# Performance work log

Hardware: AMD Instinct MI355X
Metric: run time of the kernel (lower is better)

## Reference

```python
import jax, jax.numpy as jnp
import numpy as np

B, S, D, H, F = 2, 2048, 1024, 16, 4096
DK = D // H
EPS = 1e-6


def _ln(x, g, b):
    mu = jnp.mean(x, axis=-1, keepdims=True)
    var = jnp.mean(jnp.square(x - mu), axis=-1, keepdims=True)
    return (x - mu) * jax.lax.rsqrt(var + EPS) * g + b


def setup_inputs() -> dict:
    key = jax.random.key(0)
    ks = jax.random.split(key, 8)
    sc = 0.02
    return {
        "x": jax.random.normal(ks[0], (B, S, D), jnp.float32),
        "wq": jax.random.normal(ks[1], (D, D), jnp.float32) * sc,
        "bq": jnp.zeros((D,), jnp.float32),
        "wk": jax.random.normal(ks[2], (D, D), jnp.float32) * sc,
        "bk": jnp.zeros((D,), jnp.float32),
        "wv": jax.random.normal(ks[3], (D, D), jnp.float32) * sc,
        "bv": jnp.zeros((D,), jnp.float32),
        "wo": jax.random.normal(ks[4], (D, D), jnp.float32) * sc,
        "bo": jnp.zeros((D,), jnp.float32),
        "w1": jax.random.normal(ks[5], (D, F), jnp.float32) * sc,
        "b1": jnp.zeros((F,), jnp.float32),
        "w2": jax.random.normal(ks[6], (F, D), jnp.float32) * sc,
        "b2": jnp.zeros((D,), jnp.float32),
        "g1": jnp.ones((D,), jnp.float32),
        "be1": jnp.zeros((D,), jnp.float32),
        "g2": jnp.ones((D,), jnp.float32),
        "be2": jnp.zeros((D,), jnp.float32),
    }


def reference(x, wq, bq, wk, bk, wv, bv, wo, bo, w1, b1, w2, b2, g1, be1, g2, be2):
    # Multi-head self-attention (no masks, eval-mode dropout = identity)
    q = (x @ wq + bq).reshape(B, S, H, DK)
    k = (x @ wk + bk).reshape(B, S, H, DK)
    v = (x @ wv + bv).reshape(B, S, H, DK)
    scale = 1.0 / (DK ** 0.5)
    score = jnp.einsum('bihd,bjhd->bhij', q, k) * scale  # [B,H,S,S]
    p = jax.nn.softmax(score, axis=-1)
    attn = jnp.einsum('bhij,bjhd->bihd', p, v).reshape(B, S, D)
    attn = attn @ wo + bo
    # residual + LayerNorm 1
    h = _ln(x + attn, g1, be1)
    # FFN (relu) + residual + LayerNorm 2
    ff = jax.nn.relu(h @ w1 + b1) @ w2 + b2
    return _ln(h + ff, g2, be2)
```

## Files before the change

### kernel.cpp

```cpp
#include <hip/hip_runtime.h>
#include <hip/hip_bf16.h>
#include <cmath>

typedef __bf16 bf16_t;
typedef __bf16 bf16x4 __attribute__((ext_vector_type(4)));
typedef __bf16 bf16x8 __attribute__((ext_vector_type(8)));
typedef float  f32x4  __attribute__((ext_vector_type(4)));

__device__ __forceinline__ void gld_lds16(const bf16_t* g, bf16_t* l) {
    __builtin_amdgcn_global_load_lds(
        (const __attribute__((address_space(1))) void*)g,
        (__attribute__((address_space(3))) void*)l,
        16, 0, 0);
}

struct PrepArgs {
    const float* w[6]; bf16_t* wt[6];
    int K[6], N[6], start[6];
    const float* x; bf16_t* xb; int castStart;
    const float* bq; const float* bk; float* bqkv; int biasStart;
};

__global__ __launch_bounds__(256) void prep(PrepArgs pa) {
    __shared__ float tile[32][33];
    const int bid = blockIdx.x, t = threadIdx.x;
    if (bid < pa.castStart) {
        int mi = 0;
#pragma unroll
        for (int i = 1; i < 6; i++) if (bid >= pa.start[i]) mi = i;
        const int tt  = bid - pa.start[mi];
        const int nbx = pa.N[mi] >> 5;
        const int n0 = (tt % nbx) * 32, k0 = (tt / nbx) * 32;
        const float* in = pa.w[mi];
        bf16_t* out = pa.wt[mi];
        const int K = pa.K[mi], N = pa.N[mi];
        const int tx = t & 31, ty = t >> 5;
#pragma unroll
        for (int i = 0; i < 4; i++) {
            int kk = ty + i * 8;
            tile[kk][tx] = in[(size_t)(k0 + kk) * N + n0 + tx];
        }
        __syncthreads();
#pragma unroll
        for (int i = 0; i < 4; i++) {
            int nn = ty + i * 8;
            out[(size_t)(n0 + nn) * K + k0 + tx] = (bf16_t)tile[tx][nn];
        }
    } else if (bid < pa.biasStart) {
        int i = (bid - pa.castStart) * 256 + t;
        f32x4 v = ((const f32x4*)pa.x)[i];
        bf16x4 o;
        o[0] = (bf16_t)v[0]; o[1] = (bf16_t)v[1]; o[2] = (bf16_t)v[2]; o[3] = (bf16_t)v[3];
        ((bf16x4*)pa.xb)[i] = o;
    } else {
#pragma unroll
        for (int j = 0; j < 8; j++) {
            int idx = t * 8 + j;
            pa.bqkv[idx] = idx < 1024 ? pa.bq[idx] : pa.bk[idx - 1024];
        }
    }
}

template<int MT>
__global__ __launch_bounds__(256) void gemm_bt(
    const bf16_t* __restrict__ A, const bf16_t* __restrict__ Bt,
    const float* __restrict__ bias,
    float* __restrict__ Cf, bf16_t* __restrict__ Cb,
    int M, int N, int lda, int Kloc, int relu, int nbn, int bias_row,
    long bt_bstride, long c_bstride) {
    constexpr int TM = MT * 32;
    __shared__ __attribute__((aligned(16))) bf16_t As[2][TM * 32];
    __shared__ __attribute__((aligned(16))) bf16_t Bs[2][128 * 32];
    const int tid  = threadIdx.x;
    const int lane = tid & 63;
    const int wave = tid >> 6;
    const int wm = wave & 1, wn = wave >> 1;
    const int kh = blockIdx.z;

    const int span  = 8 * nbn;
    const int group = blockIdx.x / span;
    const int rem   = blockIdx.x % span;
    const int bm    = group * 8 + (rem & 7);
    const int bn    = rem >> 3;

    const bf16_t* Bt_b = Bt + (size_t)blockIdx.y * bt_bstride;
    float*  Cf_b = Cf ? Cf + (size_t)blockIdx.y * c_bstride + (size_t)kh * M * N : nullptr;
    bf16_t* Cb_b = Cb ? Cb + (size_t)blockIdx.y * c_bstride : nullptr;
    const int koff = kh * Kloc;

    const int r4 = tid >> 2;
    const int kc = (tid & 3) * 8;
    const bf16_t* Ag = A    + (size_t)(bm * TM  + r4) * lda + koff + kc;
    const bf16_t* Bg = Bt_b + (size_t)(bn * 128 + r4) * lda + koff + kc;

    f32x4 acc[MT][4] = {};
    const int mrow = lane & 15;
    const int q8   = (lane >> 4) * 8;

    for (int k0 = 0; k0 < Kloc; k0 += 64) {
        __syncthreads();
#pragma unroll
        for (int hh = 0; hh < 2; hh++) {
#pragma unroll
            for (int i = 0; i < MT / 2; i++)
                gld_lds16(Ag + (size_t)(i * 64) * lda + k0 + hh * 32,
                          &As[hh][i * 64 * 32] + tid * 8);
            gld_lds16(Bg + k0 + hh * 32,                  &Bs[hh][0] + tid * 8);
            gld_lds16(Bg + (size_t)64 * lda + k0 + hh * 32, &Bs[hh][64 * 32] + tid * 8);
        }
        __syncthreads();

#pragma unroll
        for (int hh = 0; hh < 2; hh++) {
            bf16x8 af[MT], bfr[4];
#pragma unroll
            for (int mt = 0; mt < MT; mt++)
                af[mt] = *(const bf16x8*)(&As[hh][(wm * (MT * 16) + mt * 16 + mrow) * 32 + q8]);
#pragma unroll
            for (int nt = 0; nt < 4; nt++)
                bfr[nt] = *(const bf16x8*)(&Bs[hh][(wn * 64 + nt * 16 + mrow) * 32 + q8]);
#pragma unroll
            for (int mt = 0; mt < MT; mt++)
#pragma unroll
                for (int nt = 0; nt < 4; nt++)
                    acc[mt][nt] = __builtin_amdgcn_mfma_f32_16x16x32_bf16(
                        af[mt], bfr[nt], acc[mt][nt], 0, 0, 0);
        }
    }

    const int rq = (lane >> 4) * 4;
#pragma unroll
    for (int mt = 0; mt < MT; mt++) {
        int row0 = bm * TM + wm * (MT * 16) + mt * 16 + rq;
#pragma unroll
        for (int nt = 0; nt < 4; nt++) {
            int col = bn * 128 + wn * 64 + nt * 16 + mrow;
            float bvc = (bias && kh == 0 && !bias_row) ? bias[col] : 0.f;
#pragma unroll
            for (int r = 0; r < 4; r++) {
                float bb = (bias && kh == 0 && bias_row) ? bias[row0 + r] : bvc;
                float v = acc[mt][nt][r] + bb;
                if (relu) v = fmaxf(v, 0.f);
                size_t idx = (size_t)(row0 + r) * N + col;
                if (Cf_b) Cf_b[idx] = v;
                if (Cb_b) Cb_b[idx] = (bf16_t)v;
            }
        }
    }
}

__global__ __launch_bounds__(256) void flash_attn_mfma(
    const bf16_t* __restrict__ QKb,
    const bf16_t* __restrict__ Vtg,
    bf16_t* __restrict__ Outb) {
    __shared__ __attribute__((aligned(16))) bf16_t Ks[2][4096];
    __shared__ __attribute__((aligned(16))) bf16_t Vs[2][4096];
    __shared__ __attribute__((aligned(16))) bf16_t Ps[4096];
    const int t = threadIdx.x;
    const int lane = t & 63, wave = t >> 6;
    const int g = lane >> 4, cl = lane & 15;
    const int b = blockIdx.z, h = blockIdx.y, q0 = blockIdx.x * 64;
    const int RS = 2048;
    const bf16_t* Qg = QKb + (size_t)(b * 2048 + q0) * RS + h * 64;
    const bf16_t* Kg = QKb + (size_t)(b * 2048) * RS + 1024 + h * 64;
    const bf16_t* Vg = Vtg + ((size_t)b * 1024 + h * 64) * 2048;

    const int sr = t >> 2;
    const int sc = (t & 3) * 8;

    const bf16_t* Qrow = Qg + (size_t)(wave * 16 + cl) * RS;
    bf16x8 qr0 = *(const bf16x8*)(Qrow + g * 8);
    bf16x8 qr1 = *(const bf16x8*)(Qrow + 32 + g * 8);

    gld_lds16(Kg + (size_t)sr * RS + sc,        &Ks[0][0]    + t * 8);
    gld_lds16(Kg + (size_t)sr * RS + 32 + sc,   &Ks[0][2048] + t * 8);
    gld_lds16(Vg + (size_t)sr * 2048 + sc,      &Vs[0][0]    + t * 8);
    gld_lds16(Vg + (size_t)sr * 2048 + 32 + sc, &Vs[0][2048] + t * 8);
    __syncthreads();

    f32x4 Oacc[4] = {};
    f32x4 Lacc = {};
    bf16x8 ones;
#pragma unroll
    for (int j = 0; j < 8; j++) ones[j] = (bf16_t)1.0f;

    const int rowb = wave * 16 + cl;
    const int psw  = (cl & 7) << 4;
    char* PsB = (char*)Ps;
    const float C = 0.125f * 1.4426950408889634f;

    for (int kt_i = 0; kt_i < 32; ++kt_i) {
        const int cur = kt_i & 1;
        if (kt_i + 1 < 32) {
            const int nb  = cur ^ 1;
            const int ktn = (kt_i + 1) * 64;
            gld_lds16(Kg + (size_t)(ktn + sr) * RS + sc,        &Ks[nb][0]    + t * 8);
            gld_lds16(Kg + (size_t)(ktn + sr) * RS + 32 + sc,   &Ks[nb][2048] + t * 8);
            gld_lds16(Vg + (size_t)sr * 2048 + ktn + sc,        &Vs[nb][0]    + t * 8);
            gld_lds16(Vg + (size_t)sr * 2048 + ktn + 32 + sc,   &Vs[nb][2048] + t * 8);
        }

        f32x4 Sacc[4] = {};
#pragma unroll
        for (int ks = 0; ks < 2; ++ks) {
            bf16x8 bq = ks ? qr1 : qr0;
#pragma unroll
            for (int mt = 0; mt < 4; ++mt) {
                bf16x8 ak = *(const bf16x8*)(&Ks[cur][ks * 2048 + (mt * 16 + cl) * 32 + g * 8]);
                Sacc[mt] = __builtin_amdgcn_mfma_f32_16x16x32_bf16(ak, bq, Sacc[mt], 0, 0, 0);
            }
        }

#pragma unroll
        for (int mt = 0; mt < 4; ++mt) {
            bf16x4 p4;
#pragma unroll
            for (int r = 0; r < 4; r++)
                p4[r] = (bf16_t)__builtin_amdgcn_exp2f(Sacc[mt][r] * C);
            *(bf16x4*)(PsB + ((rowb * 128 + mt * 32 + g * 8) ^ psw)) = p4;
        }

#pragma unroll
        for (int ks = 0; ks < 2; ++ks) {
            bf16x8 ap = *(const bf16x8*)(PsB + ((rowb * 128 + ks * 64 + g * 16) ^ psw));
            Lacc = __builtin_amdgcn_mfma_f32_16x16x32_bf16(ap, ones, Lacc, 0, 0, 0);
#pragma unroll
            for (int nt = 0; nt < 4; ++nt) {
                bf16x8 bv = *(const bf16x8*)(&Vs[cur][ks * 2048 + (nt * 16 + cl) * 32 + g * 8]);
                Oacc[nt] = __builtin_amdgcn_mfma_f32_16x16x32_bf16(ap, bv, Oacc[nt], 0, 0, 0);
            }
        }

        __syncthreads();
    }

#pragma unroll
    for (int r = 0; r < 4; r++) {
        float inv = 1.f / Lacc[r];
        int qrow = q0 + wave * 16 + g * 4 + r;
        size_t base = (size_t)(b * 2048 + qrow) * 1024 + h * 64;
#pragma unroll
        for (int nt = 0; nt < 4; nt++)
            Outb[base + nt * 16 + cl] = (bf16_t)(Oacc[nt][r] * inv);
    }
}

__global__ __launch_bounds__(256) void resid_ln3(const float* __restrict__ a,
                                                 const float* __restrict__ p0,
                                                 const float* __restrict__ p1,
                                                 const float* __restrict__ g,
                                                 const float* __restrict__ be,
                                                 float* __restrict__ outf,
                                                 bf16_t* __restrict__ outb) {
    const int row = blockIdx.x, t = threadIdx.x;
    const size_t base = (size_t)row * 1024;
    f32x4 v = ((const f32x4*)(a + base))[t] + ((const f32x4*)(p0 + base))[t];
    if (p1) v += ((const f32x4*)(p1 + base))[t];
    float sum = v[0] + v[1] + v[2] + v[3];
    float sq  = v[0] * v[0] + v[1] * v[1] + v[2] * v[2] + v[3] * v[3];
#pragma unroll
    for (int o = 1; o < 64; o <<= 1) {
        sum += __shfl_xor(sum, o);
        sq  += __shfl_xor(sq, o);
    }
    __shared__ float red[8];
    int wave = t >> 6, lane = t & 63;
    if (lane == 0) { red[wave] = sum; red[4 + wave] = sq; }
    __syncthreads();
    sum = red[0] + red[1] + red[2] + red[3];
    sq  = red[4] + red[5] + red[6] + red[7];
    float mu  = sum * (1.f / 1024.f);
    float var = sq * (1.f / 1024.f) - mu * mu;
    float rs  = rsqrtf(var + 1e-6f);
    f32x4 g4 = ((const f32x4*)g)[t];
    f32x4 b4 = ((const f32x4*)be)[t];
    f32x4 o = (v - mu) * rs * g4 + b4;
    ((f32x4*)(outf + base))[t] = o;
    if (outb) {
        bf16x4 ob;
        ob[0] = (bf16_t)o[0]; ob[1] = (bf16_t)o[1]; ob[2] = (bf16_t)o[2]; ob[3] = (bf16_t)o[3];
        ((bf16x4*)(outb + base))[t] = ob;
    }
}

extern "C" void kernel_launch(void* const* d_in, const int* in_sizes, int n_in,
                              void* d_out, int out_size, void* d_ws, size_t ws_size,
                              hipStream_t stream) {
    (void)in_sizes; (void)n_in; (void)out_size; (void)ws_size;
    const float* x   = (const float*)d_in[0];
    const float* wq  = (const float*)d_in[1];
    const float* bq  = (const float*)d_in[2];
    const float* wk  = (const float*)d_in[3];
    const float* bk  = (const float*)d_in[4];
    const float* wv  = (const float*)d_in[5];
    const float* bv  = (const float*)d_in[6];
    const float* wo  = (const float*)d_in[7];
    const float* bo  = (const float*)d_in[8];
    const float* w1  = (const float*)d_in[9];
    const float* b1  = (const float*)d_in[10];
    const float* w2  = (const float*)d_in[11];
    const float* b2  = (const float*)d_in[12];
    const float* g1  = (const float*)d_in[13];
    const float* be1 = (const float*)d_in[14];
    const float* g2  = (const float*)d_in[15];
    const float* be2 = (const float*)d_in[16];
    float* out = (float*)d_out;

    char* ws = (char*)d_ws;
    const size_t MB = 1ull << 20;
    bf16_t* xb    = (bf16_t*)(ws + 0);
    bf16_t* WtQKV = (bf16_t*)(ws + 8 * MB);
    bf16_t* WtO   = (bf16_t*)(ws + 14 * MB);
    bf16_t* Wt1   = (bf16_t*)(ws + 16 * MB);
    bf16_t* Wt2   = (bf16_t*)(ws + 24 * MB);
    float*  bqkv  = (float*)(ws + 32 * MB);
    bf16_t* QKb   = (bf16_t*)(ws + 33 * MB);
    bf16_t* Vt    = (bf16_t*)(ws + 49 * MB);
    bf16_t* ffb   = (bf16_t*)(ws + 33 * MB);
    float*  oa    = (float*)(ws + 65 * MB);
    float*  f2    = (float*)(ws + 65 * MB);
    float*  hbuf  = (float*)(ws + 97 * MB);
    bf16_t* hb    = (bf16_t*)(ws + 113 * MB);
    bf16_t* ab    = xb;
    const int MN = 4096 * 1024;

    PrepArgs pa;
    pa.w[0] = wq; pa.w[1] = wk; pa.w[2] = wv; pa.w[3] = wo; pa.w[4] = w1; pa.w[5] = w2;
    pa.wt[0] = WtQKV; pa.wt[1] = WtQKV + 1024 * 1024; pa.wt[2] = WtQKV + 2048 * 1024;
    pa.wt[3] = WtO; pa.wt[4] = Wt1; pa.wt[5] = Wt2;
    int Ks[6] = {1024, 1024, 1024, 1024, 1024, 4096};
    int Ns[6] = {1024, 1024, 1024, 1024, 4096, 1024};
    int st[6] = {0, 1024, 2048, 3072, 4096, 8192};
    for (int i = 0; i < 6; i++) { pa.K[i] = Ks[i]; pa.N[i] = Ns[i]; pa.start[i] = st[i]; }
    pa.x = x; pa.xb = xb; pa.castStart = 12288;
    pa.bq = bq; pa.bk = bk; pa.bqkv = bqkv; pa.biasStart = 12288 + 4096;
    prep<<<12288 + 4096 + 1, 256, 0, stream>>>(pa);

    gemm_bt<4><<<512, 256, 0, stream>>>(xb, WtQKV, bqkv, nullptr, QKb,
                                        4096, 2048, 1024, 1024, 0, 16, 0, 0, 0);
    gemm_bt<2><<<dim3(256, 2, 1), 256, 0, stream>>>(WtQKV + 2048 * 1024, xb, bv,
                                        nullptr, Vt, 1024, 2048, 1024, 1024, 0, 16, 1,
                                        (long)2048 * 1024, (long)1024 * 2048);
    flash_attn_mfma<<<dim3(32, 16, 2), 256, 0, stream>>>(QKb, Vt, ab);
    gemm_bt<4><<<dim3(256, 1, 2), 256, 0, stream>>>(ab, WtO, bo, oa, nullptr,
                                        4096, 1024, 1024, 512, 0, 8, 0, 0, 0);
    resid_ln3<<<4096, 256, 0, stream>>>(x, oa, oa + MN, g1, be1, hbuf, hb);
    gemm_bt<4><<<1024, 256, 0, stream>>>(hb, Wt1, b1, nullptr, ffb,
                                         4096, 4096, 1024, 1024, 1, 32, 0, 0, 0);
    gemm_bt<4><<<dim3(256, 1, 2), 256, 0, stream>>>(ffb, Wt2, b2, f2, nullptr,
                                        4096, 1024, 4096, 2048, 0, 8, 0, 0, 0);
    resid_ln3<<<4096, 256, 0, stream>>>(hbuf, f2, f2 + MN, g2, be2, out, nullptr);
}
```

Before: 414.7 us.

## Double-buffer GEMM K-loop with prefetch and raise wave priority around attention MFMAs

```diff
diff --git a/kernel.cpp b/kernel.cpp
--- a/kernel.cpp
+++ b/kernel.cpp
@@ -97,35 +97,37 @@
     const int mrow = lane & 15;
     const int q8   = (lane >> 4) * 8;
 
-    for (int k0 = 0; k0 < Kloc; k0 += 64) {
+    auto stage = [&](int kk, int buf) {
+#pragma unroll
+        for (int i = 0; i < MT / 2; i++)
+            gld_lds16(Ag + (size_t)(i * 64) * lda + kk, &As[buf][i * 64 * 32] + tid * 8);
+        gld_lds16(Bg + kk,                        &Bs[buf][0] + tid * 8);
+        gld_lds16(Bg + (size_t)64 * lda + kk,     &Bs[buf][64 * 32] + tid * 8);
+    };
+
+    stage(0, 0);
+    __syncthreads();
+
+    const int nt = Kloc >> 5;
+    for (int t7 = 0; t7 < nt; ++t7) {
+        const int cur = t7 & 1;
+        if (t7 + 1 < nt) stage((t7 + 1) << 5, cur ^ 1);
+
+        bf16x8 af[MT], bfr[4];
+#pragma unroll
+        for (int mt = 0; mt < MT; mt++)
+            af[mt] = *(const bf16x8*)(&As[cur][(wm * (MT * 16) + mt * 16 + mrow) * 32 + q8]);
+#pragma unroll
+        for (int nt2 = 0; nt2 < 4; nt2++)
+            bfr[nt2] = *(const bf16x8*)(&Bs[cur][(wn * 64 + nt2 * 16 + mrow) * 32 + q8]);
+#pragma unroll
+        for (int mt = 0; mt < MT; mt++)
+#pragma unroll
+            for (int nt2 = 0; nt2 < 4; nt2++)
+                acc[mt][nt2] = __builtin_amdgcn_mfma_f32_16x16x32_bf16(
+                    af[mt], bfr[nt2], acc[mt][nt2], 0, 0, 0);
+
         __syncthreads();
-#pragma unroll
-        for (int hh = 0; hh < 2; hh++) {
-#pragma unroll
-            for (int i = 0; i < MT / 2; i++)
-                gld_lds16(Ag + (size_t)(i * 64) * lda + k0 + hh * 32,
-                          &As[hh][i * 64 * 32] + tid * 8);
-            gld_lds16(Bg + k0 + hh * 32,                  &Bs[hh][0] + tid * 8);
-            gld_lds16(Bg + (size_t)64 * lda + k0 + hh * 32, &Bs[hh][64 * 32] + tid * 8);
-        }
-        __syncthreads();
-
-#pragma unroll
-        for (int hh = 0; hh < 2; hh++) {
-            bf16x8 af[MT], bfr[4];
-#pragma unroll
-            for (int mt = 0; mt < MT; mt++)
-                af[mt] = *(const bf16x8*)(&As[hh][(wm * (MT * 16) + mt * 16 + mrow) * 32 + q8]);
-#pragma unroll
-            for (int nt = 0; nt < 4; nt++)
-                bfr[nt] = *(const bf16x8*)(&Bs[hh][(wn * 64 + nt * 16 + mrow) * 32 + q8]);
-#pragma unroll
-            for (int mt = 0; mt < MT; mt++)
-#pragma unroll
-                for (int nt = 0; nt < 4; nt++)
-                    acc[mt][nt] = __builtin_amdgcn_mfma_f32_16x16x32_bf16(
-                        af[mt], bfr[nt], acc[mt][nt], 0, 0, 0);
-        }
     }
 
     const int rq = (lane >> 4) * 4;
@@ -133,13 +135,13 @@
     for (int mt = 0; mt < MT; mt++) {
         int row0 = bm * TM + wm * (MT * 16) + mt * 16 + rq;
 #pragma unroll
-        for (int nt = 0; nt < 4; nt++) {
-            int col = bn * 128 + wn * 64 + nt * 16 + mrow;
+        for (int nt2 = 0; nt2 < 4; nt2++) {
+            int col = bn * 128 + wn * 64 + nt2 * 16 + mrow;
             float bvc = (bias && kh == 0 && !bias_row) ? bias[col] : 0.f;
 #pragma unroll
             for (int r = 0; r < 4; r++) {
                 float bb = (bias && kh == 0 && bias_row) ? bias[row0 + r] : bvc;
-                float v = acc[mt][nt][r] + bb;
+                float v = acc[mt][nt2][r] + bb;
                 if (relu) v = fmaxf(v, 0.f);
                 size_t idx = (size_t)(row0 + r) * N + col;
                 if (Cf_b) Cf_b[idx] = v;
@@ -201,6 +203,7 @@
         }
 
         f32x4 Sacc[4] = {};
+        __builtin_amdgcn_s_setprio(1);
 #pragma unroll
         for (int ks = 0; ks < 2; ++ks) {
             bf16x8 bq = ks ? qr1 : qr0;
@@ -210,6 +213,7 @@
                 Sacc[mt] = __builtin_amdgcn_mfma_f32_16x16x32_bf16(ak, bq, Sacc[mt], 0, 0, 0);
             }
         }
+        __builtin_amdgcn_s_setprio(0);
 
 #pragma unroll
         for (int mt = 0; mt < 4; ++mt) {
@@ -220,6 +224,7 @@
             *(bf16x4*)(PsB + ((rowb * 128 + mt * 32 + g * 8) ^ psw)) = p4;
         }
 
+        __builtin_amdgcn_s_setprio(1);
 #pragma unroll
         for (int ks = 0; ks < 2; ++ks) {
             bf16x8 ap = *(const bf16x8*)(PsB + ((rowb * 128 + ks * 64 + g * 16) ^ psw));
@@ -230,6 +235,7 @@
                 Oacc[nt] = __builtin_amdgcn_mfma_f32_16x16x32_bf16(ap, bv, Oacc[nt], 0, 0, 0);
             }
         }
+        __builtin_amdgcn_s_setprio(0);
 
         __syncthreads();
     }
```

Result: no change. 419.4 us (+1.1%).
